# Performance work log

Measured on AMD Instinct MI355X. Metric: run time of the kernel, lower is better.

The kernel has to match this reference:

```python
import jax, jax.numpy as jnp
import numpy as np

E = 100      # embedding_dim
FS = 5       # filter_size
HS = 6       # hidden_size (conv output spatial)
D1, D2 = 10, 10  # emb_dim1, emb_dim2
RD = E * FS * FS  # relation_dim = 2500
NE = 100000  # num_entities
NR = 500     # num_relations
B = 256      # batch
EPS = 1e-5


def _bn(x, g, b, m, v, axis):
    shape = [1] * x.ndim
    shape[axis] = x.shape[axis]
    g, b, m, v = (t.reshape(shape) for t in (g, b, m, v))
    return (x - m) * jax.lax.rsqrt(v + EPS) * g + b


def setup_inputs() -> dict:
    key = jax.random.key(0)
    ks = jax.random.split(key, 24)
    def bn_params(k, n):
        k1, k2 = jax.random.split(k)
        return (jnp.ones((n,), jnp.float32),                       # gamma
                jnp.zeros((n,), jnp.float32),                      # beta
                0.1 * jax.random.normal(k1, (n,), jnp.float32),    # running mean
                jax.random.uniform(k2, (n,), jnp.float32, 0.5, 1.5))  # running var
    bn_rel = bn_params(ks[0], RD)
    bn0 = bn_params(ks[1], 1)
    bn1 = bn_params(ks[2], E)
    bn2 = bn_params(ks[3], E)
    inp = {
        'emb_e': jax.random.normal(ks[4], (NE, E), jnp.float32),
        'emb_rel': jax.random.normal(ks[5], (NR, RD), jnp.float32) * 0.1,
        'bn_rel_g': bn_rel[0], 'bn_rel_b': bn_rel[1], 'bn_rel_m': bn_rel[2], 'bn_rel_v': bn_rel[3],
        'bn0_g': bn0[0], 'bn0_b': bn0[1], 'bn0_m': bn0[2], 'bn0_v': bn0[3],
        'bn1_g': bn1[0], 'bn1_b': bn1[1], 'bn1_m': bn1[2], 'bn1_v': bn1[3],
        'fc_w': jax.random.normal(ks[6], (E * HS * HS, E), jnp.float32) / np.sqrt(E * HS * HS),
        'fc_b': jnp.zeros((E,), jnp.float32),
        'bn2_g': bn2[0], 'bn2_b': bn2[1], 'bn2_m': bn2[2], 'bn2_v': bn2[3],
        'bias': jnp.zeros((NE,), jnp.float32),
        'e1': jax.random.randint(ks[7], (B,), 0, NE),
        'rel': jax.random.randint(ks[8], (B,), 0, NR),
    }
    return inp


def reference(emb_e, emb_rel, bn_rel_g, bn_rel_b, bn_rel_m, bn_rel_v,
              bn0_g, bn0_b, bn0_m, bn0_v, bn1_g, bn1_b, bn1_m, bn1_v,
              fc_w, fc_b, bn2_g, bn2_b, bn2_m, bn2_v, bias, e1, rel):
    # entity embedding -> (B, 1, 10, 10)
    e1_emb = emb_e[e1].reshape(B, 1, D1, D2)
    # relation embedding -> per-sample conv filters
    r = emb_rel[rel]                                   # (B, 2500)
    r = _bn(r, bn_rel_g, bn_rel_b, bn_rel_m, bn_rel_v, axis=1)
    x0 = _bn(e1_emb, bn0_g, bn0_b, bn0_m, bn0_v, axis=1)
    filters = r.reshape(B, E, FS * FS)                 # (B, 100, 25)
    # per-sample dynamic-filter conv as one batched contraction over patches
    patches = jax.lax.conv_general_dilated_patches(
        x0, (FS, FS), (1, 1), 'VALID')                 # (B, 25, 6, 6)
    x = jnp.einsum('bkhw,bck->bchw', patches, filters)  # (B, 100, 6, 6)
    x = jax.nn.relu(_bn(x, bn1_g, bn1_b, bn1_m, bn1_v, axis=1))
    x = x.reshape(B, -1)                               # (B, 3600)
    x = x @ fc_w + fc_b                                # (B, 100)
    x = jax.nn.relu(_bn(x, bn2_g, bn2_b, bn2_m, bn2_v, axis=1))
    scores = x @ emb_e.T + bias                        # (B, NE)
    return jax.nn.sigmoid(scores)
```

## Files before the change

kernel.cpp:

```cpp
#include <hip/hip_runtime.h>
#include <hip/hip_bf16.h>
#include <hip/hip_fp16.h>

#define EPS 1e-5f
#define NE_ 100000
#define B_  256

typedef _Float16 half8 __attribute__((ext_vector_type(8)));
typedef float floatx16 __attribute__((ext_vector_type(16)));

#define WS_PART  0
#define WS_H16   512000

__global__ __launch_bounds__(256) void k_convfc(
    const float* __restrict__ emb_e,
    const float* __restrict__ emb_rel,
    const float* __restrict__ bnr_g, const float* __restrict__ bnr_b,
    const float* __restrict__ bnr_m, const float* __restrict__ bnr_v,
    const float* __restrict__ bn0_g, const float* __restrict__ bn0_b,
    const float* __restrict__ bn0_m, const float* __restrict__ bn0_v,
    const float* __restrict__ bn1_g, const float* __restrict__ bn1_b,
    const float* __restrict__ bn1_m, const float* __restrict__ bn1_v,
    const float* __restrict__ fc_w,
    const int* __restrict__ e1, const int* __restrict__ rel,
    float* __restrict__ partials)
{
    __shared__ float x0s[16][100];
    __shared__ float fss[16][126];
    __shared__ float x1s[16][184];

    const int bg = blockIdx.x;
    const int ks = blockIdx.y;
    const int c0 = ks * 5;
    const int b0 = bg * 16;
    const int t  = threadIdx.x;

    const float sc0 = bn0_g[0] * rsqrtf(bn0_v[0] + EPS);
    const float sh0 = bn0_b[0] - bn0_m[0] * sc0;

    for (int idx = t; idx < 16 * 100; idx += 256) {
        int s = idx / 100, j = idx - s * 100;
        x0s[s][j] = emb_e[(size_t)e1[b0 + s] * 100 + j] * sc0 + sh0;
    }
    for (int idx = t; idx < 16 * 125; idx += 256) {
        int s = idx / 125, j = idx - s * 125;
        int g = c0 * 25 + j;
        float sc = bnr_g[g] * rsqrtf(bnr_v[g] + EPS);
        fss[s][j] = (emb_rel[(size_t)rel[b0 + s] * 2500 + g] - bnr_m[g]) * sc + bnr_b[g];
    }
    __syncthreads();

    for (int idx = t; idx < 16 * 180; idx += 256) {
        int s = idx / 180, r = idx - s * 180;
        int cl = r / 36, p = r - cl * 36;
        int hh = p / 6, ww = p - hh * 6;
        float sum = 0.f;
        #pragma unroll
        for (int ky = 0; ky < 5; ky++) {
            #pragma unroll
            for (int kx = 0; kx < 5; kx++) {
                sum += x0s[s][(hh + ky) * 10 + ww + kx] * fss[s][cl * 25 + ky * 5 + kx];
            }
        }
        int c = c0 + cl;
        float sc = bn1_g[c] * rsqrtf(bn1_v[c] + EPS);
        float y = (sum - bn1_m[c]) * sc + bn1_b[c];
        x1s[s][r] = fmaxf(y, 0.f);
    }
    __syncthreads();

    const int o  = t & 127;
    const int mg = t >> 7;
    if (o >= 100) return;

    float acc[8] = {0.f, 0.f, 0.f, 0.f, 0.f, 0.f, 0.f, 0.f};
    const float* wp = fc_w + (size_t)(c0 * 36) * 100 + o;

    for (int k0 = 0; k0 < 180; k0 += 9) {
        float wv[9];
        #pragma unroll
        for (int u = 0; u < 9; u++) wv[u] = wp[(size_t)(k0 + u) * 100];
        #pragma unroll
        for (int u = 0; u < 9; u++) {
            #pragma unroll
            for (int j = 0; j < 8; j++)
                acc[j] += x1s[mg + 2 * j][k0 + u] * wv[u];
        }
    }
    #pragma unroll
    for (int j = 0; j < 8; j++)
        partials[(size_t)ks * 25600 + (size_t)(b0 + mg + 2 * j) * 100 + o] = acc[j];
}

__global__ __launch_bounds__(256) void k_reduce(
    const float* __restrict__ partials,
    const float* __restrict__ fc_b,
    const float* __restrict__ bn2_g, const float* __restrict__ bn2_b,
    const float* __restrict__ bn2_m, const float* __restrict__ bn2_v,
    _Float16* __restrict__ h16)
{
    const int flat = blockIdx.x * 256 + threadIdx.x;
    const int b = flat / 100;
    const int o = flat - b * 100;
    float s = fc_b[o];
    #pragma unroll
    for (int ks = 0; ks < 20; ks++) s += partials[(size_t)ks * 25600 + flat];
    float sc = bn2_g[o] * rsqrtf(bn2_v[o] + EPS);
    float y = (s - bn2_m[o]) * sc + bn2_b[o];
    y = fmaxf(y, 0.f);
    h16[((o >> 3) * 256 + b) * 8 + (o & 7)] = (_Float16)y;
    if (o < 12) {
        int kp = 100 + o;
        h16[((kp >> 3) * 256 + b) * 8 + (kp & 7)] = (_Float16)0.f;
    }
}

__global__ __launch_bounds__(256) void k_scores(
    const float* __restrict__ emb_e,
    const float* __restrict__ bias,
    const _Float16* __restrict__ h16,
    float* __restrict__ out)
{
    const int t    = threadIdx.x;
    const int wave = t >> 6;
    const int lane = t & 63;
    const int l31  = lane & 31;
    const int hf   = lane >> 5;

    const int n0 = blockIdx.x * 128 + wave * 32;

    const int e  = n0 + l31;
    const int el = (e < NE_) ? e : (NE_ - 1);
    const float* erow = emb_e + (size_t)el * 100;

    half8 bf[7];
    #pragma unroll
    for (int kc = 0; kc < 7; kc++) {
        const int k0 = kc * 16 + hf * 8;
        half8 h;
        if (k0 + 8 <= 100) {
            const float4 f0 = *(const float4*)(erow + k0);
            const float4 f1 = *(const float4*)(erow + k0 + 4);
            h[0] = (_Float16)f0.x; h[1] = (_Float16)f0.y;
            h[2] = (_Float16)f0.z; h[3] = (_Float16)f0.w;
            h[4] = (_Float16)f1.x; h[5] = (_Float16)f1.y;
            h[6] = (_Float16)f1.z; h[7] = (_Float16)f1.w;
        } else if (k0 < 100) {
            const float4 f0 = *(const float4*)(erow + k0);
            h[0] = (_Float16)f0.x; h[1] = (_Float16)f0.y;
            h[2] = (_Float16)f0.z; h[3] = (_Float16)f0.w;
            h[4] = (_Float16)0.f; h[5] = (_Float16)0.f;
            h[6] = (_Float16)0.f; h[7] = (_Float16)0.f;
        } else {
            #pragma unroll
            for (int j = 0; j < 8; j++) h[j] = (_Float16)0.f;
        }
        bf[kc] = h;
    }

    const half8* hA = (const half8*)h16;
    const float bb = (e < NE_) ? bias[e] : 0.f;

    #pragma unroll 2
    for (int mt = 0; mt < 8; mt++) {
        floatx16 acc;
        #pragma unroll
        for (int r = 0; r < 16; r++) acc[r] = 0.f;

        const int m = mt * 32 + l31;
        #pragma unroll
        for (int kc = 0; kc < 7; kc++) {
            const half8 a = hA[(kc * 2 + hf) * 256 + m];
            acc = __builtin_amdgcn_mfma_f32_32x32x16_f16(a, bf[kc], acc, 0, 0, 0);
        }

        if (e < NE_) {
            #pragma unroll
            for (int r = 0; r < 16; r++) {
                const int row = mt * 32 + (r & 3) + 8 * (r >> 2) + 4 * hf;
                const float v = 1.f / (1.f + __expf(-(acc[r] + bb)));
                __builtin_nontemporal_store(v, &out[(size_t)row * NE_ + e]);
            }
        }
    }
}

extern "C" void kernel_launch(void* const* d_in, const int* in_sizes, int n_in,
                              void* d_out, int out_size, void* d_ws, size_t ws_size,
                              hipStream_t stream) {
    const float* emb_e   = (const float*)d_in[0];
    const float* emb_rel = (const float*)d_in[1];
    const float* bnr_g   = (const float*)d_in[2];
    const float* bnr_b   = (const float*)d_in[3];
    const float* bnr_m   = (const float*)d_in[4];
    const float* bnr_v   = (const float*)d_in[5];
    const float* bn0_g   = (const float*)d_in[6];
    const float* bn0_b   = (const float*)d_in[7];
    const float* bn0_m   = (const float*)d_in[8];
    const float* bn0_v   = (const float*)d_in[9];
    const float* bn1_g   = (const float*)d_in[10];
    const float* bn1_b   = (const float*)d_in[11];
    const float* bn1_m   = (const float*)d_in[12];
    const float* bn1_v   = (const float*)d_in[13];
    const float* fc_w    = (const float*)d_in[14];
    const float* fc_b    = (const float*)d_in[15];
    const float* bn2_g   = (const float*)d_in[16];
    const float* bn2_b   = (const float*)d_in[17];
    const float* bn2_m   = (const float*)d_in[18];
    const float* bn2_v   = (const float*)d_in[19];
    const float* bias    = (const float*)d_in[20];
    const int* e1  = (const int*)d_in[21];
    const int* rel = (const int*)d_in[22];

    float* ws       = (float*)d_ws;
    float* partials = ws + WS_PART;
    _Float16* h16   = (_Float16*)(ws + WS_H16);

    k_convfc<<<dim3(16, 20), dim3(256), 0, stream>>>(
        emb_e, emb_rel,
        bnr_g, bnr_b, bnr_m, bnr_v,
        bn0_g, bn0_b, bn0_m, bn0_v,
        bn1_g, bn1_b, bn1_m, bn1_v,
        fc_w, e1, rel, partials);

    k_reduce<<<dim3(100), dim3(256), 0, stream>>>(
        partials, fc_b, bn2_g, bn2_b, bn2_m, bn2_v, h16);

    k_scores<<<dim3((NE_ + 127) / 128), dim3(256), 0, stream>>>(
        emb_e, bias, h16, (float*)d_out);
}
```

Before: 225.5 us.

## Stage entity rows through LDS with coalesced loads; halve convfc batch tile

The scores kernel now loads each block's 128 entity rows with fully coalesced float4 reads into shared memory, converting to fp16 in MFMA fragment layout, instead of each lane reading its own 400-byte row strided in global memory. The conv/fc kernel processes 8 samples per block instead of 16, doubling the grid to 640 blocks for better occupancy across CUs. The trade-offs are extra LDS traffic plus a barrier in the scores kernel, and more redundant fc_w reads in convfc.

```diff
diff --git a/kernel.cpp b/kernel.cpp
--- a/kernel.cpp
+++ b/kernel.cpp
@@ -25,24 +25,24 @@
     const int* __restrict__ e1, const int* __restrict__ rel,
     float* __restrict__ partials)
 {
-    __shared__ float x0s[16][100];
-    __shared__ float fss[16][126];
-    __shared__ float x1s[16][184];
+    __shared__ float x0s[8][100];
+    __shared__ float fss[8][126];
+    __shared__ float x1s[8][184];
 
     const int bg = blockIdx.x;
     const int ks = blockIdx.y;
     const int c0 = ks * 5;
-    const int b0 = bg * 16;
+    const int b0 = bg * 8;
     const int t  = threadIdx.x;
 
     const float sc0 = bn0_g[0] * rsqrtf(bn0_v[0] + EPS);
     const float sh0 = bn0_b[0] - bn0_m[0] * sc0;
 
-    for (int idx = t; idx < 16 * 100; idx += 256) {
+    for (int idx = t; idx < 8 * 100; idx += 256) {
         int s = idx / 100, j = idx - s * 100;
         x0s[s][j] = emb_e[(size_t)e1[b0 + s] * 100 + j] * sc0 + sh0;
     }
-    for (int idx = t; idx < 16 * 125; idx += 256) {
+    for (int idx = t; idx < 8 * 125; idx += 256) {
         int s = idx / 125, j = idx - s * 125;
         int g = c0 * 25 + j;
         float sc = bnr_g[g] * rsqrtf(bnr_v[g] + EPS);
@@ -50,7 +50,7 @@
     }
     __syncthreads();
 
-    for (int idx = t; idx < 16 * 180; idx += 256) {
+    for (int idx = t; idx < 8 * 180; idx += 256) {
         int s = idx / 180, r = idx - s * 180;
         int cl = r / 36, p = r - cl * 36;
         int hh = p / 6, ww = p - hh * 6;
@@ -73,7 +73,7 @@
     const int mg = t >> 7;
     if (o >= 100) return;
 
-    float acc[8] = {0.f, 0.f, 0.f, 0.f, 0.f, 0.f, 0.f, 0.f};
+    float acc[4] = {0.f, 0.f, 0.f, 0.f};
     const float* wp = fc_w + (size_t)(c0 * 36) * 100 + o;
 
     for (int k0 = 0; k0 < 180; k0 += 9) {
@@ -83,12 +83,12 @@
         #pragma unroll
         for (int u = 0; u < 9; u++) {
             #pragma unroll
-            for (int j = 0; j < 8; j++)
+            for (int j = 0; j < 4; j++)
                 acc[j] += x1s[mg + 2 * j][k0 + u] * wv[u];
         }
     }
     #pragma unroll
-    for (int j = 0; j < 8; j++)
+    for (int j = 0; j < 4; j++)
         partials[(size_t)ks * 25600 + (size_t)(b0 + mg + 2 * j) * 100 + o] = acc[j];
 }
 
@@ -121,6 +121,8 @@
     const _Float16* __restrict__ h16,
     float* __restrict__ out)
 {
+    __shared__ _Float16 ebf[4 * 14 * 32 * 8];
+
     const int t    = threadIdx.x;
     const int wave = t >> 6;
     const int lane = t & 63;
@@ -128,34 +130,43 @@
     const int hf   = lane >> 5;
 
     const int n0 = blockIdx.x * 128 + wave * 32;
-
     const int e  = n0 + l31;
-    const int el = (e < NE_) ? e : (NE_ - 1);
-    const float* erow = emb_e + (size_t)el * 100;
+
+    {
+        const size_t gbase = (size_t)blockIdx.x * 12800;
+        for (int f0 = t * 4; f0 < 12800; f0 += 1024) {
+            const size_t gf = gbase + f0;
+            float4 v;
+            if (gf + 4 <= (size_t)NE_ * 100) {
+                v = *(const float4*)(emb_e + gf);
+            } else {
+                v = make_float4(0.f, 0.f, 0.f, 0.f);
+            }
+            #pragma unroll
+            for (int i = 0; i < 4; i++) {
+                const int f = f0 + i;
+                const int r = f / 100;
+                const int k = f - r * 100;
+                const int chunk = (r >> 5) * 14 + (k >> 4) * 2 + ((k >> 3) & 1);
+                const float fv = (i == 0) ? v.x : (i == 1) ? v.y : (i == 2) ? v.z : v.w;
+                ebf[chunk * 256 + (r & 31) * 8 + (k & 7)] = (_Float16)fv;
+            }
+        }
+        for (int idx = t; idx < 128 * 12; idx += 256) {
+            const int r  = idx / 12;
+            const int kp = 100 + (idx - r * 12);
+            const int chunk = (r >> 5) * 14 + (kp >> 4) * 2 + ((kp >> 3) & 1);
+            ebf[chunk * 256 + (r & 31) * 8 + (kp & 7)] = (_Float16)0.f;
+        }
+    }
+    __syncthreads();
 
     half8 bf[7];
-    #pragma unroll
-    for (int kc = 0; kc < 7; kc++) {
-        const int k0 = kc * 16 + hf * 8;
-        half8 h;
-        if (k0 + 8 <= 100) {
-            const float4 f0 = *(const float4*)(erow + k0);
-            const float4 f1 = *(const float4*)(erow + k0 + 4);
-            h[0] = (_Float16)f0.x; h[1] = (_Float16)f0.y;
-            h[2] = (_Float16)f0.z; h[3] = (_Float16)f0.w;
-            h[4] = (_Float16)f1.x; h[5] = (_Float16)f1.y;
-            h[6] = (_Float16)f1.z; h[7] = (_Float16)f1.w;
-        } else if (k0 < 100) {
-            const float4 f0 = *(const float4*)(erow + k0);
-            h[0] = (_Float16)f0.x; h[1] = (_Float16)f0.y;
-            h[2] = (_Float16)f0.z; h[3] = (_Float16)f0.w;
-            h[4] = (_Float16)0.f; h[5] = (_Float16)0.f;
-            h[6] = (_Float16)0.f; h[7] = (_Float16)0.f;
-        } else {
-            #pragma unroll
-            for (int j = 0; j < 8; j++) h[j] = (_Float16)0.f;
-        }
-        bf[kc] = h;
+    {
+        const half8* eb8 = (const half8*)ebf;
+        #pragma unroll
+        for (int kc = 0; kc < 7; kc++)
+            bf[kc] = eb8[(wave * 14 + kc * 2 + hf) * 32 + l31];
     }
 
     const half8* hA = (const half8*)h16;
@@ -216,7 +227,7 @@
     float* partials = ws + WS_PART;
     _Float16* h16   = (_Float16*)(ws + WS_H16);
 
-    k_convfc<<<dim3(16, 20), dim3(256), 0, stream>>>(
+    k_convfc<<<dim3(32, 20), dim3(256), 0, stream>>>(
         emb_e, emb_rel,
         bnr_g, bnr_b, bnr_m, bnr_v,
         bn0_g, bn0_b, bn0_m, bn0_v,
```

New measurement: 218.1 us. 1.03x faster.
